# Performance work log

Hardware: AMD Instinct MI355X
Metric: run time of the kernel (lower is better)

## Reference

```python
import jax, jax.numpy as jnp
import numpy as np

B, S, D_IN, D_H = 8, 4096, 256, 512
EPS = 1e-6


def setup_inputs() -> dict:
    key = jax.random.key(0)
    ks = jax.random.split(key, 5)
    scale = 1.0 / np.sqrt(D_IN)  # torch Linear default init scale (uniform bound)
    x = jax.random.normal(ks[0], (B, S, D_IN), dtype=jnp.float32)
    Wi = jax.random.normal(ks[1], (D_IN, D_H), dtype=jnp.float32) * scale
    Wf = jax.random.normal(ks[2], (D_IN, D_H), dtype=jnp.float32) * scale
    Wo = jax.random.normal(ks[3], (D_IN, D_H), dtype=jnp.float32) * scale
    Wz = jax.random.normal(ks[4], (D_IN, D_H), dtype=jnp.float32) * scale
    zb = jnp.zeros((D_H,), dtype=jnp.float32)
    return {"x": x, "Wi": Wi, "bi": zb, "Wf": Wf, "bf": zb,
            "Wo": Wo, "bo": zb, "Wz": Wz, "bz": zb}


def _xlstm_forward(x, Wi, bi, Wf, bf, Wo, bo, Wz, bz):
    # Batched projections over all timesteps at once: [B,S,D_H] each.
    i_t = jnp.exp(jnp.clip(jnp.einsum('bsd,dh->bsh', x, Wi) + bi, -20.0, 0.0))
    f_t = jnp.exp(jnp.clip(jnp.einsum('bsd,dh->bsh', x, Wf) + bf, -20.0, 0.0))
    o_t = jax.nn.sigmoid(jnp.einsum('bsd,dh->bsh', x, Wo) + bo)
    z_t = jnp.tanh(jnp.einsum('bsd,dh->bsh', x, Wz) + bz)

    def step(carry, gates):
        c, n = carry
        i, f, o, z = gates
        c = f * c + i * z
        n = f * n + i
        h = o * (c / (n + EPS))
        return (c, n), h

    c0 = jnp.zeros((x.shape[0], Wi.shape[1]), dtype=x.dtype)
    n0 = jnp.ones((x.shape[0], Wi.shape[1]), dtype=x.dtype)
    # time-major scan over the recurrence
    gates_tm = tuple(jnp.swapaxes(g, 0, 1) for g in (i_t, f_t, o_t, z_t))  # [S,B,H]
    _, h_tm = jax.lax.scan(step, (c0, n0), gates_tm)
    return jnp.swapaxes(h_tm, 0, 1)  # [B,S,H]


def reference(x, Wi, bi, Wf, bf, Wo, bo, Wz, bz):
    return _xlstm_forward(x, Wi, bi, Wf, bf, Wo, bo, Wz, bz)
```

## Files before the change

### kernel.cpp

```cpp
#include <hip/hip_runtime.h>
#include <hip/hip_bf16.h>
#include <cstdint>
#include <cstddef>

typedef __hip_bfloat16 bf16;
typedef __attribute__((ext_vector_type(8))) short short8;
typedef __attribute__((ext_vector_type(4))) short short4v;
typedef __attribute__((ext_vector_type(4))) float floatx4;

#define BB 8
#define SS 4096
#define DIN 256
#define DH 512
#define NCH 128
#define CHUNK 32

__device__ __forceinline__ float b2f(bf16 v) { return __bfloat162float(v); }
__device__ __forceinline__ float sh2f(short v) {
    unsigned int u = ((unsigned int)(unsigned short)v) << 16;
    float f; __builtin_memcpy(&f, &u, 4); return f;
}
__device__ __forceinline__ float frcp(float x) { return __builtin_amdgcn_rcpf(x); }

__global__ __launch_bounds__(256) void convert_x(
    const float* __restrict__ X, bf16* __restrict__ Xb)
{
    const int idx = blockIdx.x * 256 + threadIdx.x;
    float4 v = ((const float4*)X)[idx];
    bf16 o[4] = {__float2bfloat16(v.x), __float2bfloat16(v.y),
                 __float2bfloat16(v.z), __float2bfloat16(v.w)};
    ((short4v*)Xb)[idx] = *(const short4v*)o;
}

__global__ __launch_bounds__(256) void transpose_w(
    const float* __restrict__ Wi, const float* __restrict__ Wf,
    const float* __restrict__ Wo, const float* __restrict__ Wz,
    bf16* __restrict__ Wt)
{
    int o  = blockIdx.x * 256 + threadIdx.x;
    int nf = o >> 8;
    int k  = o & 255;
    int g  = nf >> 9;
    int hh = nf & 511;
    const float* W = (g == 0) ? Wi : (g == 1) ? Wf : (g == 2) ? Wo : Wz;
    Wt[o] = __float2bfloat16(W[(size_t)k * DH + hh]);
}

__device__ __forceinline__ void load16_lds(const bf16* g, short* l)
{
    __builtin_amdgcn_global_load_lds(
        (const __attribute__((address_space(1))) unsigned int*)g,
        (__attribute__((address_space(3))) unsigned int*)l,
        16, 0, 0);
}

__global__ __launch_bounds__(256) void gemm_mfma(
    const bf16* __restrict__ Xb, const bf16* __restrict__ Wt,
    const float* __restrict__ bi, const float* __restrict__ bfv,
    const float* __restrict__ bo, const float* __restrict__ bz,
    bf16* __restrict__ Pi, bf16* __restrict__ Pf,
    bf16* __restrict__ Po, bf16* __restrict__ Pz)
{
    __shared__ __align__(16) short As[128 * 32];
    __shared__ __align__(16) short Bs[128 * 32];

    const int tid  = threadIdx.x;
    const int m0   = blockIdx.x * 128;
    const int n0   = blockIdx.y * 128;
    const int wave = tid >> 6, lane = tid & 63;
    const int wm   = (wave >> 1) * 64, wn = (wave & 1) * 64;
    const int l15  = lane & 15;
    const int q    = lane >> 4;

    floatx4 acc[4][4];
#pragma unroll
    for (int i = 0; i < 4; i++)
#pragma unroll
        for (int j = 0; j < 4; j++) acc[i][j] = (floatx4){0.f, 0.f, 0.f, 0.f};

    const int r_ld = tid >> 2;
    const int c_ld = tid & 3;
    const bf16* agp0 = Xb + (size_t)(m0 + r_ld) * DIN + c_ld * 8;
    const bf16* agp1 = Xb + (size_t)(m0 + 64 + r_ld) * DIN + c_ld * 8;
    const bf16* bgp0 = Wt + (size_t)(n0 + r_ld) * DIN + c_ld * 8;
    const bf16* bgp1 = Wt + (size_t)(n0 + 64 + r_ld) * DIN + c_ld * 8;

    for (int k0 = 0; k0 < DIN; k0 += 32) {
        load16_lds(agp0 + k0, &As[tid * 8]);
        load16_lds(agp1 + k0, &As[2048 + tid * 8]);
        load16_lds(bgp0 + k0, &Bs[tid * 8]);
        load16_lds(bgp1 + k0, &Bs[2048 + tid * 8]);
        __syncthreads();

        short8 af[4], bfr[4];
#pragma unroll
        for (int ti = 0; ti < 4; ti++)
            af[ti] = *(const short8*)&As[(wm + ti * 16 + l15) * 32 + q * 8];
#pragma unroll
        for (int tj = 0; tj < 4; tj++)
            bfr[tj] = *(const short8*)&Bs[(wn + tj * 16 + l15) * 32 + q * 8];
#pragma unroll
        for (int ti = 0; ti < 4; ti++)
#pragma unroll
            for (int tj = 0; tj < 4; tj++)
                acc[ti][tj] = __builtin_amdgcn_mfma_f32_16x16x32_bf16(
                    af[ti], bfr[tj], acc[ti][tj], 0, 0, 0);
        __syncthreads();
    }

    const int g = n0 >> 9;
    const float* bias = (g == 0) ? bi : (g == 1) ? bfv : (g == 2) ? bo : bz;
    bf16* pb = (g == 0) ? Pi : (g == 1) ? Pf : (g == 2) ? Po : Pz;

#pragma unroll
    for (int ti = 0; ti < 4; ti++) {
        const int mrow = m0 + wm + ti * 16 + q * 4;
#pragma unroll
        for (int tj = 0; tj < 4; tj++) {
            const int hh = (n0 + wn + tj * 16 + l15) & 511;
            const float bsv = bias[hh];
#pragma unroll
            for (int r = 0; r < 4; r++) {
                const float v = acc[ti][tj][r] + bsv;
                float a;
                if (g == 0 || g == 1) {
                    a = __expf(fminf(fmaxf(v, -20.f), 0.f));
                } else if (g == 2) {
                    a = frcp(1.f + __expf(-v));
                } else {
                    a = 1.f - 2.f * frcp(__expf(2.f * v) + 1.f);
                }
                pb[(size_t)(mrow + r) * DH + hh] = __float2bfloat16(a);
            }
        }
    }
}

__global__ __launch_bounds__(256) void scan_carry(
    const bf16* __restrict__ Pi, const bf16* __restrict__ Pf,
    const bf16* __restrict__ Pz,
    float* __restrict__ Aa, float* __restrict__ Bca, float* __restrict__ Bna,
    int nb)
{
    const int tid = threadIdx.x;
    const int ch  = blockIdx.x * 4 + (tid >> 6);
    const int b   = blockIdx.y;
    const int hg  = (tid & 63) * 8;
    const size_t base = ((size_t)(b * SS + ch * CHUNK)) * DH + hg;

    float A[8], Bc[8], Bn[8];
#pragma unroll
    for (int j = 0; j < 8; j++) { A[j] = 1.f; Bc[j] = 0.f; Bn[j] = 0.f; }

#pragma unroll 4
    for (int s = 0; s < CHUNK; s++) {
        const size_t o = base + (size_t)s * DH;
        short8 i8 = *(const short8*)(Pi + o);
        short8 f8 = *(const short8*)(Pf + o);
        short8 z8 = *(const short8*)(Pz + o);
#pragma unroll
        for (int j = 0; j < 8; j++) {
            const float f  = sh2f(f8[j]);
            const float iv = sh2f(i8[j]);
            const float zv = sh2f(z8[j]);
            Bc[j] = fmaf(f, Bc[j], iv * zv);
            Bn[j] = fmaf(f, Bn[j], iv);
            A[j] *= f;
        }
    }
    const size_t cidx = (size_t)(ch * nb + b) * DH + hg;
#pragma unroll
    for (int j = 0; j < 2; j++) {
        *(floatx4*)(Aa  + cidx + j * 4) = *(floatx4*)&A[j * 4];
        *(floatx4*)(Bca + cidx + j * 4) = *(floatx4*)&Bc[j * 4];
        *(floatx4*)(Bna + cidx + j * 4) = *(floatx4*)&Bn[j * 4];
    }
}

__global__ __launch_bounds__(256) void scan_chunks(
    const float* __restrict__ Aa, const float* __restrict__ Bca,
    const float* __restrict__ Bna,
    float* __restrict__ Cs, float* __restrict__ Ns, int nb)
{
    const int t = blockIdx.x * 256 + threadIdx.x;
    float c = 0.f, n = 1.f;
    for (int ch = 0; ch < NCH; ch++) {
        const size_t cidx = (size_t)ch * (nb * DH) + t;
        Cs[cidx] = c; Ns[cidx] = n;
        const float A = Aa[cidx];
        c = fmaf(A, c, Bca[cidx]);
        n = fmaf(A, n, Bna[cidx]);
    }
}

__global__ __launch_bounds__(256) void scan_emit(
    const bf16* __restrict__ Pi, const bf16* __restrict__ Pf,
    const bf16* __restrict__ Po, const bf16* __restrict__ Pz,
    const float* __restrict__ Cs, const float* __restrict__ Ns,
    float* __restrict__ out, int nb)
{
    const int tid = threadIdx.x;
    const int ch  = blockIdx.x * 4 + (tid >> 6);
    const int b   = blockIdx.y;
    const int hg  = (tid & 63) * 8;
    const size_t base = ((size_t)(b * SS + ch * CHUNK)) * DH + hg;
    const size_t cidx = (size_t)(ch * nb + b) * DH + hg;

    float c[8], n[8];
#pragma unroll
    for (int j = 0; j < 2; j++) {
        *(floatx4*)&c[j * 4] = *(const floatx4*)(Cs + cidx + j * 4);
        *(floatx4*)&n[j * 4] = *(const floatx4*)(Ns + cidx + j * 4);
    }

#pragma unroll 4
    for (int s = 0; s < CHUNK; s++) {
        const size_t o = base + (size_t)s * DH;
        short8 i8 = *(const short8*)(Pi + o);
        short8 f8 = *(const short8*)(Pf + o);
        short8 o8 = *(const short8*)(Po + o);
        short8 z8 = *(const short8*)(Pz + o);
        float h[8];
#pragma unroll
        for (int j = 0; j < 8; j++) {
            const float f  = sh2f(f8[j]);
            const float iv = sh2f(i8[j]);
            const float ov = sh2f(o8[j]);
            const float zv = sh2f(z8[j]);
            c[j] = fmaf(f, c[j], iv * zv);
            n[j] = fmaf(f, n[j], iv);
            h[j] = ov * c[j] * frcp(n[j] + 1e-6f);
        }
        *(floatx4*)(out + o)     = *(floatx4*)&h[0];
        *(floatx4*)(out + o + 4) = *(floatx4*)&h[4];
    }
}

extern "C" void kernel_launch(void* const* d_in, const int* in_sizes, int n_in,
                              void* d_out, int out_size, void* d_ws, size_t ws_size,
                              hipStream_t stream)
{
    const float* x   = (const float*)d_in[0];
    const float* Wi  = (const float*)d_in[1];
    const float* bi  = (const float*)d_in[2];
    const float* Wf  = (const float*)d_in[3];
    const float* bfv = (const float*)d_in[4];
    const float* Wo  = (const float*)d_in[5];
    const float* bo  = (const float*)d_in[6];
    const float* Wz  = (const float*)d_in[7];
    const float* bz  = (const float*)d_in[8];
    float* out = (float*)d_out;

    int nb = BB;
    while (nb > 1) {
        size_t need = (1u << 20)
                    + (size_t)nb * SS * DIN * 2
                    + 4 * (size_t)nb * SS * DH * 2
                    + 5 * (size_t)NCH * nb * DH * 4;
        if (need <= ws_size) break;
        nb >>= 1;
    }

    const size_t plane = (size_t)nb * SS * DH;
    bf16* Wt = (bf16*)d_ws;
    bf16* Xb = (bf16*)((char*)d_ws + (1u << 20));
    bf16* Pi = Xb + (size_t)nb * SS * DIN;
    bf16* Pf = Pi + plane;
    bf16* Po = Pf + plane;
    bf16* Pz = Po + plane;
    float* Aa  = (float*)(Pz + plane);
    float* Bca = Aa  + (size_t)NCH * nb * DH;
    float* Bna = Bca + (size_t)NCH * nb * DH;
    float* Cs  = Bna + (size_t)NCH * nb * DH;
    float* Ns  = Cs  + (size_t)NCH * nb * DH;

    transpose_w<<<2048, 256, 0, stream>>>(Wi, Wf, Wo, Wz, Wt);

    for (int b0 = 0; b0 < BB; b0 += nb) {
        const float* Xsrc = x   + (size_t)b0 * SS * DIN;
        float*       Ob   = out + (size_t)b0 * SS * DH;
        convert_x<<<nb * 1024, 256, 0, stream>>>(Xsrc, Xb);
        gemm_mfma<<<dim3(nb * SS / 128, 16), 256, 0, stream>>>(
            Xb, Wt, bi, bfv, bo, bz, Pi, Pf, Po, Pz);
        scan_carry<<<dim3(NCH / 4, nb), 256, 0, stream>>>(
            Pi, Pf, Pz, Aa, Bca, Bna, nb);
        scan_chunks<<<2 * nb, 256, 0, stream>>>(Aa, Bca, Bna, Cs, Ns, nb);
        scan_emit<<<dim3(NCH / 4, nb), 256, 0, stream>>>(
            Pi, Pf, Po, Pz, Cs, Ns, Ob, nb);
    }
}
```

Measured before the change: 244.5 us.

## Fuse chunk carry computation into GEMM epilogue via interleaved gate columns

```diff
diff --git a/kernel.cpp b/kernel.cpp
--- a/kernel.cpp
+++ b/kernel.cpp
@@ -21,6 +21,10 @@
     float f; __builtin_memcpy(&f, &u, 4); return f;
 }
 __device__ __forceinline__ float frcp(float x) { return __builtin_amdgcn_rcpf(x); }
+__device__ __forceinline__ short f2sh(float a) {
+    bf16 bv = __float2bfloat16(a);
+    short sv; __builtin_memcpy(&sv, &bv, 2); return sv;
+}
 
 __global__ __launch_bounds__(256) void convert_x(
     const float* __restrict__ X, bf16* __restrict__ Xb)
@@ -37,13 +41,15 @@
     const float* __restrict__ Wo, const float* __restrict__ Wz,
     bf16* __restrict__ Wt)
 {
-    int o  = blockIdx.x * 256 + threadIdx.x;
-    int nf = o >> 8;
-    int k  = o & 255;
-    int g  = nf >> 9;
-    int hh = nf & 511;
+    int o = blockIdx.x * 256 + threadIdx.x;
+    int r = o >> 8;
+    int k = o & 255;
+    int y = r >> 7;
+    int c = r & 127;
+    int g = c >> 5;
+    int h = y * 32 + (c & 31);
     const float* W = (g == 0) ? Wi : (g == 1) ? Wf : (g == 2) ? Wo : Wz;
-    Wt[o] = __float2bfloat16(W[(size_t)k * DH + hh]);
+    Wt[o] = __float2bfloat16(W[(size_t)k * DH + h]);
 }
 
 __device__ __forceinline__ void load16_lds(const bf16* g, short* l)
@@ -59,14 +65,18 @@
     const float* __restrict__ bi, const float* __restrict__ bfv,
     const float* __restrict__ bo, const float* __restrict__ bz,
     bf16* __restrict__ Pi, bf16* __restrict__ Pf,
-    bf16* __restrict__ Po, bf16* __restrict__ Pz)
-{
-    __shared__ __align__(16) short As[128 * 32];
-    __shared__ __align__(16) short Bs[128 * 32];
+    bf16* __restrict__ Po, bf16* __restrict__ Pz,
+    float* __restrict__ Aa, float* __restrict__ Bca, float* __restrict__ Bna,
+    int nb)
+{
+    __shared__ __align__(16) short smem[128 * 132];
+    short* As = smem;
+    short* Bs = smem + 4096;
 
     const int tid  = threadIdx.x;
     const int m0   = blockIdx.x * 128;
-    const int n0   = blockIdx.y * 128;
+    const int y    = blockIdx.y;
+    const int n0   = y * 128;
     const int wave = tid >> 6, lane = tid & 63;
     const int wm   = (wave >> 1) * 64, wn = (wave & 1) * 64;
     const int l15  = lane & 15;
@@ -108,17 +118,17 @@
         __syncthreads();
     }
 
-    const int g = n0 >> 9;
-    const float* bias = (g == 0) ? bi : (g == 1) ? bfv : (g == 2) ? bo : bz;
-    bf16* pb = (g == 0) ? Pi : (g == 1) ? Pf : (g == 2) ? Po : Pz;
-
 #pragma unroll
     for (int ti = 0; ti < 4; ti++) {
-        const int mrow = m0 + wm + ti * 16 + q * 4;
+        const int mrow = wm + ti * 16 + q * 4;
 #pragma unroll
         for (int tj = 0; tj < 4; tj++) {
-            const int hh = (n0 + wn + tj * 16 + l15) & 511;
-            const float bsv = bias[hh];
+            const int cb = wn + tj * 16;
+            const int g  = cb >> 5;
+            const int c  = cb + l15;
+            const float* bp = (g == 0) ? bi : (g == 1) ? bfv
+                            : (g == 2) ? bo : bz;
+            const float bsv = bp[y * 32 + (c & 31)];
 #pragma unroll
             for (int r = 0; r < 4; r++) {
                 const float v = acc[ti][tj][r] + bsv;
@@ -130,50 +140,47 @@
                 } else {
                     a = 1.f - 2.f * frcp(__expf(2.f * v) + 1.f);
                 }
-                pb[(size_t)(mrow + r) * DH + hh] = __float2bfloat16(a);
+                smem[(mrow + r) * 132 + c] = f2sh(a);
             }
         }
     }
-}
-
-__global__ __launch_bounds__(256) void scan_carry(
-    const bf16* __restrict__ Pi, const bf16* __restrict__ Pf,
-    const bf16* __restrict__ Pz,
-    float* __restrict__ Aa, float* __restrict__ Bca, float* __restrict__ Bna,
-    int nb)
-{
-    const int tid = threadIdx.x;
-    const int ch  = blockIdx.x * 4 + (tid >> 6);
-    const int b   = blockIdx.y;
-    const int hg  = (tid & 63) * 8;
-    const size_t base = ((size_t)(b * SS + ch * CHUNK)) * DH + hg;
-
-    float A[8], Bc[8], Bn[8];
-#pragma unroll
-    for (int j = 0; j < 8; j++) { A[j] = 1.f; Bc[j] = 0.f; Bn[j] = 0.f; }
-
-#pragma unroll 4
-    for (int s = 0; s < CHUNK; s++) {
-        const size_t o = base + (size_t)s * DH;
-        short8 i8 = *(const short8*)(Pi + o);
-        short8 f8 = *(const short8*)(Pf + o);
-        short8 z8 = *(const short8*)(Pz + o);
-#pragma unroll
-        for (int j = 0; j < 8; j++) {
-            const float f  = sh2f(f8[j]);
-            const float iv = sh2f(i8[j]);
-            const float zv = sh2f(z8[j]);
-            Bc[j] = fmaf(f, Bc[j], iv * zv);
-            Bn[j] = fmaf(f, Bn[j], iv);
-            A[j] *= f;
-        }
-    }
-    const size_t cidx = (size_t)(ch * nb + b) * DH + hg;
-#pragma unroll
-    for (int j = 0; j < 2; j++) {
-        *(floatx4*)(Aa  + cidx + j * 4) = *(floatx4*)&A[j * 4];
-        *(floatx4*)(Bca + cidx + j * 4) = *(floatx4*)&Bc[j * 4];
-        *(floatx4*)(Bna + cidx + j * 4) = *(floatx4*)&Bn[j * 4];
+    __syncthreads();
+
+    const int bidx = m0 / SS;
+
+    {
+        const int cp  = (tid & 31) * 4;
+        const int g2  = cp >> 5;
+        const int hb  = y * 32 + (cp & 31);
+        bf16* pl = ((g2 == 0) ? Pi : (g2 == 1) ? Pf : (g2 == 2) ? Po : Pz) + hb;
+        const int r0 = tid >> 5;
+#pragma unroll
+        for (int t = 0; t < 16; t++) {
+            const int row = t * 8 + r0;
+            short4v v = *(const short4v*)&smem[row * 132 + cp];
+            *(short4v*)(pl + (size_t)(m0 + row) * DH) = v;
+        }
+    }
+
+    if (tid < 128) {
+        const int hh = tid & 31;
+        const int ch = tid >> 5;
+        float A = 1.f, Bc = 0.f, Bn = 0.f;
+        const short* base = &smem[(ch * 32) * 132];
+#pragma unroll 8
+        for (int s = 0; s < CHUNK; s++) {
+            const short* rp = base + s * 132;
+            const float iv = sh2f(rp[hh]);
+            const float f  = sh2f(rp[32 + hh]);
+            const float zv = sh2f(rp[96 + hh]);
+            Bc = fmaf(f, Bc, iv * zv);
+            Bn = fmaf(f, Bn, iv);
+            A *= f;
+        }
+        const int ch_g = ((m0 % SS) >> 5) + ch;
+        const int hgl  = y * 32 + hh;
+        const size_t cidx = (size_t)(ch_g * nb + bidx) * DH + hgl;
+        Aa[cidx] = A; Bca[cidx] = Bc; Bna[cidx] = Bn;
     }
 }
 
@@ -281,9 +288,7 @@
         float*       Ob   = out + (size_t)b0 * SS * DH;
         convert_x<<<nb * 1024, 256, 0, stream>>>(Xsrc, Xb);
         gemm_mfma<<<dim3(nb * SS / 128, 16), 256, 0, stream>>>(
-            Xb, Wt, bi, bfv, bo, bz, Pi, Pf, Po, Pz);
-        scan_carry<<<dim3(NCH / 4, nb), 256, 0, stream>>>(
-            Pi, Pf, Pz, Aa, Bca, Bna, nb);
+            Xb, Wt, bi, bfv, bo, bz, Pi, Pf, Po, Pz, Aa, Bca, Bna, nb);
         scan_chunks<<<2 * nb, 256, 0, stream>>>(Aa, Bca, Bna, Cs, Ns, nb);
         scan_emit<<<dim3(NCH / 4, nb), 256, 0, stream>>>(
             Pi, Pf, Po, Pz, Cs, Ns, Ob, nb);
```

Measured after the change: 237.6 us. 1.03x faster.
